# Kernel optimization log

Hardware: AMD Instinct MI355X
Metric: run time of the kernel (lower is better)

Reference implementation:

```python
import jax, jax.numpy as jnp
import numpy as np

D_MODEL = 1024
N_HEADS = 16
D_K = D_MODEL // N_HEADS


def setup_inputs() -> dict:
    key = jax.random.key(0)
    ks = jax.random.split(key, 9)
    s = 0.02
    x = jax.random.normal(ks[0], (2, 2048, D_MODEL), dtype=jnp.float32)
    Wq = jax.random.normal(ks[1], (D_MODEL, D_MODEL), dtype=jnp.float32) * s
    bq = jax.random.normal(ks[2], (D_MODEL,), dtype=jnp.float32) * s
    Wk = jax.random.normal(ks[3], (D_MODEL, D_MODEL), dtype=jnp.float32) * s
    bk = jax.random.normal(ks[4], (D_MODEL,), dtype=jnp.float32) * s
    Wv = jax.random.normal(ks[5], (D_MODEL, D_MODEL), dtype=jnp.float32) * s
    bv = jax.random.normal(ks[6], (D_MODEL,), dtype=jnp.float32) * s
    Wo = jax.random.normal(ks[7], (D_MODEL, D_MODEL), dtype=jnp.float32) * s
    bo = jax.random.normal(ks[8], (D_MODEL,), dtype=jnp.float32) * s
    return {"x": x, "Wq": Wq, "bq": bq, "Wk": Wk, "bk": bk,
            "Wv": Wv, "bv": bv, "Wo": Wo, "bo": bo}


def reference(x, Wq, bq, Wk, bk, Wv, bv, Wo, bo):
    B, S, D = x.shape
    # nn.Linear: y = x @ W.T + b
    q = x @ Wq.T + bq  # [B,S,D]
    k = x @ Wk.T + bk
    v = x @ Wv.T + bv
    # split heads -> [B,H,S,dk]
    q = q.reshape(B, S, N_HEADS, D_K).transpose(0, 2, 1, 3)
    k = k.reshape(B, S, N_HEADS, D_K).transpose(0, 2, 1, 3)
    v = v.reshape(B, S, N_HEADS, D_K).transpose(0, 2, 1, 3)
    scale = 1.0 / jnp.sqrt(jnp.asarray(D_K, dtype=x.dtype))
    scores = jnp.einsum('bhqd,bhkd->bhqk', q, k) * scale  # [B,H,S,S]
    weights = jax.nn.softmax(scores, axis=-1)
    out = jnp.einsum('bhqk,bhkd->bhqd', weights, v)  # [B,H,S,dk]
    concat = out.transpose(0, 2, 1, 3).reshape(B, S, D)
    return concat @ Wo.T + bo
```

## Files before the change

### kernel.cpp

```cpp
#include <hip/hip_runtime.h>

typedef unsigned short ushort_t;
typedef __attribute__((ext_vector_type(8))) __bf16 bf16x8;
typedef __attribute__((ext_vector_type(4))) float floatx4;

#define AS1 __attribute__((address_space(1)))
#define AS3 __attribute__((address_space(3)))

#define D_MODEL 1024
#define NH 16
#define DKH 64
#define SEQ 2048
#define NB 2
#define MTOT (NB * SEQ)

#define QSCALE 0.18033688011112042f

#define OFF_X   0u
#define OFF_WQ  4194304u
#define OFF_BQ  5242880u
#define OFF_WK  5243904u
#define OFF_BK  6292480u
#define OFF_WV  6293504u
#define OFF_BV  7342080u
#define OFF_WO  7343104u
#define OFF_BO  8391680u
#define CVT_TOT 8392704u

__device__ __forceinline__ float bf2f(ushort_t u) {
    union { unsigned u; float f; } v; v.u = ((unsigned)u) << 16; return v.f;
}
__device__ __forceinline__ ushort_t f2bf(float f) {
    union { float f; unsigned u; } v; v.f = f;
    unsigned r = v.u + 0x7FFFu + ((v.u >> 16) & 1u);
    return (ushort_t)(r >> 16);
}
__device__ __forceinline__ unsigned pack2bf(float a, float b) {
    unsigned ua = __float_as_uint(a), ub = __float_as_uint(b);
    ua = ua + 0x7FFFu + ((ua >> 16) & 1u);
    ub = ub + 0x7FFFu + ((ub >> 16) & 1u);
    return __builtin_amdgcn_perm(ub, ua, 0x07060302);
}

__global__ __launch_bounds__(256) void convert_kernel(
    const float* __restrict__ x,  const float* __restrict__ wq, const float* __restrict__ bq_,
    const float* __restrict__ wk, const float* __restrict__ bk_, const float* __restrict__ wv,
    const float* __restrict__ bv_, const float* __restrict__ wo, const float* __restrict__ bo_,
    ushort_t* __restrict__ dst)
{
    const unsigned idx = ((unsigned)blockIdx.x * 256u + threadIdx.x) * 4u;
    if (idx >= CVT_TOT) return;
    const float* src; unsigned off;
    if      (idx < OFF_WQ) { src = x;   off = idx; }
    else if (idx < OFF_BQ) { src = wq;  off = idx - OFF_WQ; }
    else if (idx < OFF_WK) { src = bq_; off = idx - OFF_BQ; }
    else if (idx < OFF_BK) { src = wk;  off = idx - OFF_WK; }
    else if (idx < OFF_WV) { src = bk_; off = idx - OFF_BK; }
    else if (idx < OFF_BV) { src = wv;  off = idx - OFF_WV; }
    else if (idx < OFF_WO) { src = bv_; off = idx - OFF_BV; }
    else if (idx < OFF_BO) { src = wo;  off = idx - OFF_WO; }
    else                   { src = bo_; off = idx - OFF_BO; }
    float4 v = *reinterpret_cast<const float4*>(src + off);
    uint2 p;
    p.x = pack2bf(v.x, v.y);
    p.y = pack2bf(v.z, v.w);
    *reinterpret_cast<uint2*>(dst + idx) = p;
}

__device__ __forceinline__ void gemm_core(
    const ushort_t* __restrict__ X, const ushort_t* __restrict__ W,
    int m0, int n0, ushort_t* As, ushort_t* Bs, floatx4 acc[4][4])
{
    const int tid = threadIdx.x;
    const int lane = tid & 63, wv = tid >> 6;
    const int wm = (wv >> 1) * 64, wn = (wv & 1) * 64;
    const int l15 = lane & 15, quad = lane >> 4;
    const floatx4 z4 = {0.f, 0.f, 0.f, 0.f};
#pragma unroll
    for (int i = 0; i < 4; ++i)
#pragma unroll
        for (int j = 0; j < 4; ++j) acc[i][j] = z4;
    const int lrow = lane >> 2;
    const int lcol = (lane & 3) * 8;
    const ushort_t* gA = X + (size_t)(m0 + lrow) * D_MODEL + lcol;
    const ushort_t* gB = W + (size_t)(n0 + lrow) * D_MODEL + lcol;
    for (int k0 = 0; k0 < D_MODEL; k0 += 32) {
        __syncthreads();
#pragma unroll
        for (int j = 0; j < 2; ++j) {
            const int r0 = (wv * 2 + j) * 16;
            __builtin_amdgcn_global_load_lds(
                (const AS1 unsigned*)(gA + (size_t)r0 * D_MODEL + k0),
                (AS3 unsigned*)(As + r0 * 32), 16, 0, 0);
            __builtin_amdgcn_global_load_lds(
                (const AS1 unsigned*)(gB + (size_t)r0 * D_MODEL + k0),
                (AS3 unsigned*)(Bs + r0 * 32), 16, 0, 0);
        }
        asm volatile("s_waitcnt vmcnt(0)" ::: "memory");
        __syncthreads();
        bf16x8 af[4], bfr[4];
#pragma unroll
        for (int i = 0; i < 4; ++i)
            af[i] = *reinterpret_cast<const bf16x8*>(As + (wm + i * 16 + l15) * 32 + quad * 8);
#pragma unroll
        for (int j = 0; j < 4; ++j)
            bfr[j] = *reinterpret_cast<const bf16x8*>(Bs + (wn + j * 16 + l15) * 32 + quad * 8);
#pragma unroll
        for (int i = 0; i < 4; ++i)
#pragma unroll
            for (int j = 0; j < 4; ++j)
                acc[i][j] = __builtin_amdgcn_mfma_f32_16x16x32_bf16(af[i], bfr[j], acc[i][j], 0, 0, 0);
    }
}

__global__ __launch_bounds__(256, 3) void qkv_kernel(
    const ushort_t* __restrict__ x,
    const ushort_t* __restrict__ Wq, const ushort_t* __restrict__ bq,
    const ushort_t* __restrict__ Wk, const ushort_t* __restrict__ bk,
    const ushort_t* __restrict__ Wv, const ushort_t* __restrict__ bv,
    ushort_t* __restrict__ q_ws, ushort_t* __restrict__ k_ws, ushort_t* __restrict__ vt_ws)
{
    __shared__ __align__(16) ushort_t lds[17408];
    ushort_t* As = lds;
    ushort_t* Bs = lds + 128 * 32;
    const int m0 = blockIdx.x * 128;
    const int which = blockIdx.y >> 3;
    const int n0 = (blockIdx.y & 7) * 128;
    const ushort_t* W    = (which == 0) ? Wq : (which == 1) ? Wk : Wv;
    const ushort_t* bias = (which == 0) ? bq : (which == 1) ? bk : bv;
    floatx4 acc[4][4];
    gemm_core(x, W, m0, n0, As, Bs, acc);
    const int tid = threadIdx.x, lane = tid & 63, wv = tid >> 6;
    const int wm = (wv >> 1) * 64, wn = (wv & 1) * 64;
    const int l15 = lane & 15, quad = lane >> 4;
    const int b0 = m0 >> 11;
    const int s0 = m0 & (SEQ - 1);
    __syncthreads();
    if (which < 2) {
        ushort_t* Ts = lds;
        ushort_t* dst = (which == 0) ? q_ws : k_ws;
        const float scl = (which == 0) ? QSCALE : 1.0f;
#pragma unroll
        for (int j = 0; j < 4; ++j) {
            int coln = wn + j * 16 + l15;
            float bb = bf2f(bias[n0 + coln]);
#pragma unroll
            for (int i = 0; i < 4; ++i)
#pragma unroll
                for (int r = 0; r < 4; ++r) {
                    int rowm = wm + i * 16 + quad * 4 + r;
                    Ts[rowm * 136 + coln] = f2bf((acc[i][j][r] + bb) * scl);
                }
        }
        __syncthreads();
#pragma unroll
        for (int i = 0; i < 8; ++i) {
            int c = tid + 256 * i;
            int rowm = c >> 4, chunk = c & 15;
            float4 v = *reinterpret_cast<const float4*>(Ts + rowm * 136 + chunk * 8);
            int s = s0 + rowm;
            int n = n0 + chunk * 8, h = n >> 6, d = n & 63;
            *reinterpret_cast<float4*>(dst + (((size_t)(b0 * NH + h)) * SEQ + s) * DKH + d) = v;
        }
    } else {
        ushort_t* Ts = lds;
#pragma unroll
        for (int j = 0; j < 4; ++j) {
            int coln = wn + j * 16 + l15;
            float bb = bf2f(bias[n0 + coln]);
#pragma unroll
            for (int i = 0; i < 4; ++i)
#pragma unroll
                for (int r = 0; r < 4; ++r) {
                    int rowm = wm + i * 16 + quad * 4 + r;
                    Ts[coln * 136 + rowm] = f2bf(acc[i][j][r] + bb);
                }
        }
        __syncthreads();
#pragma unroll
        for (int i = 0; i < 8; ++i) {
            int c = tid + 256 * i;
            int nr = c >> 4, mc = (c & 15) * 8;
            float4 v = *reinterpret_cast<const float4*>(Ts + nr * 136 + mc);
            int n = n0 + nr, h = n >> 6, d = n & 63;
            *reinterpret_cast<float4*>(vt_ws + (((size_t)(b0 * NH + h)) * DKH + d) * SEQ + s0 + mc) = v;
        }
    }
}

__global__ __launch_bounds__(512, 4) void attn_kernel(
    const ushort_t* __restrict__ q_ws, const ushort_t* __restrict__ k_ws,
    const ushort_t* __restrict__ vt_ws, ushort_t* __restrict__ concat)
{
    __shared__ __align__(16) ushort_t sm[36864];
    const int qb = blockIdx.x, bh = blockIdx.y;
    const int tid = threadIdx.x;
    const int lane = tid & 63, wv = tid >> 6;
    const int half = wv >> 2, wq = wv & 3;
    const int l15 = lane & 15, quad = lane >> 4;
    const int ht = tid & 255;

    const ushort_t* Qg = q_ws + ((size_t)bh * SEQ + qb * 128) * DKH;
    const ushort_t* Kg = k_ws + ((size_t)bh * SEQ + half * (SEQ / 2)) * DKH;
    const ushort_t* Vg = vt_ws + (size_t)bh * DKH * SEQ + half * (SEQ / 2);

    ushort_t* Ks     = sm + half * 4608;
    ushort_t* VTs    = sm + 9216 + half * 4608;
    ushort_t* Ps     = sm + 18432 + wv * 2304;
    ushort_t* Qstage = sm + 18432;

#pragma unroll
    for (int i = 0; i < 2; ++i) {
        int c = tid + 512 * i;
        int row = c >> 3, col = (c & 7) * 8;
        *reinterpret_cast<float4*>(Qstage + row * 72 + col) =
            *reinterpret_cast<const float4*>(Qg + row * DKH + col);
    }
    __syncthreads();
    bf16x8 aq[2][2];
#pragma unroll
    for (int nt = 0; nt < 2; ++nt)
#pragma unroll
        for (int ks = 0; ks < 2; ++ks)
            aq[nt][ks] = *reinterpret_cast<const bf16x8*>(Qstage + (wq * 32 + nt * 16 + l15) * 72 + ks * 32 + quad * 8);

    const floatx4 z4 = {0.f, 0.f, 0.f, 0.f};
    floatx4 o[2][4];
    float lacc[2] = {0.f, 0.f};
#pragma unroll
    for (int nt = 0; nt < 2; ++nt)
#pragma unroll
        for (int dt = 0; dt < 4; ++dt) o[nt][dt] = z4;

    for (int t = 0; t < 16; ++t) {
        __syncthreads();
#pragma unroll
        for (int i = 0; i < 2; ++i) {
            int c = ht + 256 * i;
            int row = c >> 3, col = (c & 7) * 8;
            *reinterpret_cast<float4*>(Ks + row * 72 + col) =
                *reinterpret_cast<const float4*>(Kg + (size_t)(t * 64 + row) * DKH + col);
            *reinterpret_cast<float4*>(VTs + row * 72 + col) =
                *reinterpret_cast<const float4*>(Vg + (size_t)row * SEQ + t * 64 + col);
        }
        __syncthreads();

        floatx4 st[2][4];
#pragma unroll
        for (int nt = 0; nt < 2; ++nt)
#pragma unroll
            for (int mt = 0; mt < 4; ++mt) st[nt][mt] = z4;
#pragma unroll
        for (int ks = 0; ks < 2; ++ks)
#pragma unroll
            for (int mt = 0; mt < 4; ++mt) {
                bf16x8 akf = *reinterpret_cast<const bf16x8*>(Ks + (mt * 16 + l15) * 72 + ks * 32 + quad * 8);
                st[0][mt] = __builtin_amdgcn_mfma_f32_16x16x32_bf16(akf, aq[0][ks], st[0][mt], 0, 0, 0);
                st[1][mt] = __builtin_amdgcn_mfma_f32_16x16x32_bf16(akf, aq[1][ks], st[1][mt], 0, 0, 0);
            }

#pragma unroll
        for (int nt = 0; nt < 2; ++nt)
#pragma unroll
            for (int mt = 0; mt < 4; ++mt)
#pragma unroll
                for (int r = 0; r < 4; ++r) {
                    float p = exp2f(st[nt][mt][r]);
                    st[nt][mt][r] = p;
                    lacc[nt] += p;
                }
#pragma unroll
        for (int nt = 0; nt < 2; ++nt)
#pragma unroll
            for (int mt = 0; mt < 4; ++mt) {
                uint2 pk;
                pk.x = pack2bf(st[nt][mt][0], st[nt][mt][1]);
                pk.y = pack2bf(st[nt][mt][2], st[nt][mt][3]);
                *reinterpret_cast<uint2*>(Ps + (nt * 16 + l15) * 72 + mt * 16 + quad * 4) = pk;
            }
        asm volatile("s_waitcnt lgkmcnt(0)" ::: "memory");
#pragma unroll
        for (int ks = 0; ks < 2; ++ks) {
            bf16x8 ap0 = *reinterpret_cast<const bf16x8*>(Ps + l15 * 72 + ks * 32 + quad * 8);
            bf16x8 ap1 = *reinterpret_cast<const bf16x8*>(Ps + (16 + l15) * 72 + ks * 32 + quad * 8);
#pragma unroll
            for (int dt = 0; dt < 4; ++dt) {
                bf16x8 bvv = *reinterpret_cast<const bf16x8*>(VTs + (dt * 16 + l15) * 72 + ks * 32 + quad * 8);
                o[0][dt] = __builtin_amdgcn_mfma_f32_16x16x32_bf16(ap0, bvv, o[0][dt], 0, 0, 0);
                o[1][dt] = __builtin_amdgcn_mfma_f32_16x16x32_bf16(ap1, bvv, o[1][dt], 0, 0, 0);
            }
        }
    }
#pragma unroll
    for (int nt = 0; nt < 2; ++nt) {
        lacc[nt] += __shfl_xor(lacc[nt], 16, 64);
        lacc[nt] += __shfl_xor(lacc[nt], 32, 64);
    }
    __syncthreads();
    float* Of = (float*)sm;
    float* lf = Of + 128 * 68;
    if (half == 1) {
#pragma unroll
        for (int nt = 0; nt < 2; ++nt) {
            if (quad == 0) lf[wq * 32 + nt * 16 + l15] = lacc[nt];
#pragma unroll
            for (int r = 0; r < 4; ++r) {
                int row = wq * 32 + nt * 16 + quad * 4 + r;
#pragma unroll
                for (int dt = 0; dt < 4; ++dt)
                    Of[row * 68 + dt * 16 + l15] = o[nt][dt][r];
            }
        }
    }
    __syncthreads();
    if (half == 0) {
        const int b0 = bh >> 4, h = bh & 15;
#pragma unroll
        for (int nt = 0; nt < 2; ++nt) {
            float ltot = lacc[nt] + lf[wq * 32 + nt * 16 + l15];
            float linv = 1.f / ltot;
#pragma unroll
            for (int r = 0; r < 4; ++r) {
                float lB = __shfl(linv, quad * 4 + r, 64);
                int row = wq * 32 + nt * 16 + quad * 4 + r;
                size_t base = ((size_t)(b0 * SEQ + qb * 128 + row)) * D_MODEL + h * DKH;
#pragma unroll
                for (int dt = 0; dt < 4; ++dt) {
                    float sum = o[nt][dt][r] + Of[row * 68 + dt * 16 + l15];
                    concat[base + dt * 16 + l15] = f2bf(sum * lB);
                }
            }
        }
    }
}

__global__ __launch_bounds__(256, 3) void oproj_kernel(
    const ushort_t* __restrict__ cc, const ushort_t* __restrict__ Wo,
    const ushort_t* __restrict__ bo, float* __restrict__ out)
{
    __shared__ __align__(16) ushort_t lds[2 * 128 * 32];
    ushort_t* As = lds;
    ushort_t* Bs = lds + 128 * 32;
    const int m0 = blockIdx.x * 128, n0 = blockIdx.y * 128;
    floatx4 acc[4][4];
    gemm_core(cc, Wo, m0, n0, As, Bs, acc);
    const int tid = threadIdx.x, lane = tid & 63, wv = tid >> 6;
    const int wm = (wv >> 1) * 64, wn = (wv & 1) * 64;
    const int l15 = lane & 15, quad = lane >> 4;
#pragma unroll
    for (int j = 0; j < 4; ++j) {
        int n = n0 + wn + j * 16 + l15;
        float bb = bf2f(bo[n]);
#pragma unroll
        for (int i = 0; i < 4; ++i)
#pragma unroll
            for (int r = 0; r < 4; ++r) {
                int m = m0 + wm + i * 16 + quad * 4 + r;
                out[(size_t)m * D_MODEL + n] = acc[i][j][r] + bb;
            }
    }
}

extern "C" void kernel_launch(void* const* d_in, const int* in_sizes, int n_in,
                              void* d_out, int out_size, void* d_ws, size_t ws_size,
                              hipStream_t stream)
{
    ushort_t* cvt = (ushort_t*)d_ws;
    const ushort_t* xb  = cvt + OFF_X;
    const ushort_t* Wqb = cvt + OFF_WQ;
    const ushort_t* bqb = cvt + OFF_BQ;
    const ushort_t* Wkb = cvt + OFF_WK;
    const ushort_t* bkb = cvt + OFF_BK;
    const ushort_t* Wvb = cvt + OFF_WV;
    const ushort_t* bvb = cvt + OFF_BV;
    const ushort_t* Wob = cvt + OFF_WO;
    const ushort_t* bob = cvt + OFF_BO;
    ushort_t* q_ws   = cvt + CVT_TOT;
    ushort_t* k_ws   = q_ws  + (size_t)MTOT * D_MODEL;
    ushort_t* vt_ws  = k_ws  + (size_t)MTOT * D_MODEL;
    ushort_t* concat = vt_ws + (size_t)MTOT * D_MODEL;

    convert_kernel<<<(CVT_TOT / 1024), 256, 0, stream>>>(
        (const float*)d_in[0], (const float*)d_in[1], (const float*)d_in[2],
        (const float*)d_in[3], (const float*)d_in[4], (const float*)d_in[5],
        (const float*)d_in[6], (const float*)d_in[7], (const float*)d_in[8], cvt);
    qkv_kernel<<<dim3(32, 24), 256, 0, stream>>>(xb, Wqb, bqb, Wkb, bkb, Wvb, bvb, q_ws, k_ws, vt_ws);
    attn_kernel<<<dim3(16, 32), 512, 0, stream>>>(q_ws, k_ws, vt_ws, concat);
    oproj_kernel<<<dim3(32, 8), 256, 0, stream>>>(concat, Wob, bob, (float*)d_out);
}
```

Measured before the change: 210.2 us.

## Keep softmax probabilities in registers, shrink attention blocks, deepen GEMM K-step

Attention now feeds the exponentiated scores straight from the score accumulators into a 16x16x16 MFMA as the B operand with V^T as A, so the LDS round trip for P is gone. Attention blocks shrink to 256 threads and 64 queries with a grid of 32x32, and Q is loaded straight from global memory instead of through LDS staging. The QKV and output-projection GEMMs load a 64-wide K slab per barrier, halving the number of syncs at the cost of twice the LDS per block. The epilogue transposes the partial-output exchange layout so concat writes become packed 4-element stores.

```diff
diff --git a/kernel.cpp b/kernel.cpp
--- a/kernel.cpp
+++ b/kernel.cpp
@@ -2,6 +2,7 @@
 
 typedef unsigned short ushort_t;
 typedef __attribute__((ext_vector_type(8))) __bf16 bf16x8;
+typedef __attribute__((ext_vector_type(4))) short short4v;
 typedef __attribute__((ext_vector_type(4))) float floatx4;
 
 #define AS1 __attribute__((address_space(1)))
@@ -27,6 +28,8 @@
 #define OFF_BO  8391680u
 #define CVT_TOT 8392704u
 
+#define MFMA16(a, b, c) __builtin_amdgcn_mfma_f32_16x16x16bf16_1k((a), (b), (c), 0, 0, 0)
+
 __device__ __forceinline__ float bf2f(ushort_t u) {
     union { unsigned u; float f; } v; v.u = ((unsigned)u) << 16; return v.f;
 }
@@ -40,6 +43,12 @@
     ua = ua + 0x7FFFu + ((ua >> 16) & 1u);
     ub = ub + 0x7FFFu + ((ub >> 16) & 1u);
     return __builtin_amdgcn_perm(ub, ua, 0x07060302);
+}
+__device__ __forceinline__ short4v pack4bf(floatx4 v) {
+    union { uint2 u; short4v s; } cv;
+    cv.u.x = pack2bf(v[0], v[1]);
+    cv.u.y = pack2bf(v[2], v[3]);
+    return cv.s;
 }
 
 __global__ __launch_bounds__(256) void convert_kernel(
@@ -69,7 +78,7 @@
 
 __device__ __forceinline__ void gemm_core(
     const ushort_t* __restrict__ X, const ushort_t* __restrict__ W,
-    int m0, int n0, ushort_t* As, ushort_t* Bs, floatx4 acc[4][4])
+    int m0, int n0, ushort_t* lds, floatx4 acc[4][4])
 {
     const int tid = threadIdx.x;
     const int lane = tid & 63, wv = tid >> 6;
@@ -84,32 +93,43 @@
     const int lcol = (lane & 3) * 8;
     const ushort_t* gA = X + (size_t)(m0 + lrow) * D_MODEL + lcol;
     const ushort_t* gB = W + (size_t)(n0 + lrow) * D_MODEL + lcol;
-    for (int k0 = 0; k0 < D_MODEL; k0 += 32) {
+    for (int k0 = 0; k0 < D_MODEL; k0 += 64) {
         __syncthreads();
 #pragma unroll
         for (int j = 0; j < 2; ++j) {
             const int r0 = (wv * 2 + j) * 16;
             __builtin_amdgcn_global_load_lds(
                 (const AS1 unsigned*)(gA + (size_t)r0 * D_MODEL + k0),
-                (AS3 unsigned*)(As + r0 * 32), 16, 0, 0);
+                (AS3 unsigned*)(lds + r0 * 32), 16, 0, 0);
+            __builtin_amdgcn_global_load_lds(
+                (const AS1 unsigned*)(gA + (size_t)r0 * D_MODEL + k0 + 32),
+                (AS3 unsigned*)(lds + 4096 + r0 * 32), 16, 0, 0);
             __builtin_amdgcn_global_load_lds(
                 (const AS1 unsigned*)(gB + (size_t)r0 * D_MODEL + k0),
-                (AS3 unsigned*)(Bs + r0 * 32), 16, 0, 0);
+                (AS3 unsigned*)(lds + 8192 + r0 * 32), 16, 0, 0);
+            __builtin_amdgcn_global_load_lds(
+                (const AS1 unsigned*)(gB + (size_t)r0 * D_MODEL + k0 + 32),
+                (AS3 unsigned*)(lds + 12288 + r0 * 32), 16, 0, 0);
         }
         asm volatile("s_waitcnt vmcnt(0)" ::: "memory");
         __syncthreads();
-        bf16x8 af[4], bfr[4];
-#pragma unroll
-        for (int i = 0; i < 4; ++i)
-            af[i] = *reinterpret_cast<const bf16x8*>(As + (wm + i * 16 + l15) * 32 + quad * 8);
-#pragma unroll
-        for (int j = 0; j < 4; ++j)
-            bfr[j] = *reinterpret_cast<const bf16x8*>(Bs + (wn + j * 16 + l15) * 32 + quad * 8);
-#pragma unroll
-        for (int i = 0; i < 4; ++i)
+#pragma unroll
+        for (int ks = 0; ks < 2; ++ks) {
+            const ushort_t* A = lds + ks * 4096;
+            const ushort_t* B = lds + 8192 + ks * 4096;
+            bf16x8 af[4], bfr[4];
+#pragma unroll
+            for (int i = 0; i < 4; ++i)
+                af[i] = *reinterpret_cast<const bf16x8*>(A + (wm + i * 16 + l15) * 32 + quad * 8);
 #pragma unroll
             for (int j = 0; j < 4; ++j)
-                acc[i][j] = __builtin_amdgcn_mfma_f32_16x16x32_bf16(af[i], bfr[j], acc[i][j], 0, 0, 0);
+                bfr[j] = *reinterpret_cast<const bf16x8*>(B + (wn + j * 16 + l15) * 32 + quad * 8);
+#pragma unroll
+            for (int i = 0; i < 4; ++i)
+#pragma unroll
+                for (int j = 0; j < 4; ++j)
+                    acc[i][j] = __builtin_amdgcn_mfma_f32_16x16x32_bf16(af[i], bfr[j], acc[i][j], 0, 0, 0);
+        }
     }
 }
 
@@ -121,15 +141,13 @@
     ushort_t* __restrict__ q_ws, ushort_t* __restrict__ k_ws, ushort_t* __restrict__ vt_ws)
 {
     __shared__ __align__(16) ushort_t lds[17408];
-    ushort_t* As = lds;
-    ushort_t* Bs = lds + 128 * 32;
     const int m0 = blockIdx.x * 128;
     const int which = blockIdx.y >> 3;
     const int n0 = (blockIdx.y & 7) * 128;
     const ushort_t* W    = (which == 0) ? Wq : (which == 1) ? Wk : Wv;
     const ushort_t* bias = (which == 0) ? bq : (which == 1) ? bk : bv;
     floatx4 acc[4][4];
-    gemm_core(x, W, m0, n0, As, Bs, acc);
+    gemm_core(x, W, m0, n0, lds, acc);
     const int tid = threadIdx.x, lane = tid & 63, wv = tid >> 6;
     const int wm = (wv >> 1) * 64, wn = (wv & 1) * 64;
     const int l15 = lane & 15, quad = lane >> 4;
@@ -188,45 +206,36 @@
     }
 }
 
-__global__ __launch_bounds__(512, 4) void attn_kernel(
+__global__ __launch_bounds__(256, 4) void attn_kernel(
     const ushort_t* __restrict__ q_ws, const ushort_t* __restrict__ k_ws,
     const ushort_t* __restrict__ vt_ws, ushort_t* __restrict__ concat)
 {
-    __shared__ __align__(16) ushort_t sm[36864];
+    __shared__ __align__(16) ushort_t sm[18432];
     const int qb = blockIdx.x, bh = blockIdx.y;
     const int tid = threadIdx.x;
     const int lane = tid & 63, wv = tid >> 6;
-    const int half = wv >> 2, wq = wv & 3;
+    const int half = wv >> 1, wq = wv & 1;
     const int l15 = lane & 15, quad = lane >> 4;
-    const int ht = tid & 255;
-
-    const ushort_t* Qg = q_ws + ((size_t)bh * SEQ + qb * 128) * DKH;
+    const int ht = tid & 127;
+
+    const ushort_t* Qg = q_ws + ((size_t)bh * SEQ + qb * 64) * DKH;
     const ushort_t* Kg = k_ws + ((size_t)bh * SEQ + half * (SEQ / 2)) * DKH;
     const ushort_t* Vg = vt_ws + (size_t)bh * DKH * SEQ + half * (SEQ / 2);
 
-    ushort_t* Ks     = sm + half * 4608;
-    ushort_t* VTs    = sm + 9216 + half * 4608;
-    ushort_t* Ps     = sm + 18432 + wv * 2304;
-    ushort_t* Qstage = sm + 18432;
-
-#pragma unroll
-    for (int i = 0; i < 2; ++i) {
-        int c = tid + 512 * i;
-        int row = c >> 3, col = (c & 7) * 8;
-        *reinterpret_cast<float4*>(Qstage + row * 72 + col) =
-            *reinterpret_cast<const float4*>(Qg + row * DKH + col);
-    }
-    __syncthreads();
+    ushort_t* Ks  = sm + half * 4608;
+    ushort_t* VTs = sm + 9216 + half * 4608;
+
     bf16x8 aq[2][2];
 #pragma unroll
     for (int nt = 0; nt < 2; ++nt)
 #pragma unroll
         for (int ks = 0; ks < 2; ++ks)
-            aq[nt][ks] = *reinterpret_cast<const bf16x8*>(Qstage + (wq * 32 + nt * 16 + l15) * 72 + ks * 32 + quad * 8);
+            aq[nt][ks] = *reinterpret_cast<const bf16x8*>(
+                Qg + (size_t)(wq * 32 + nt * 16 + l15) * DKH + ks * 32 + quad * 8);
 
     const floatx4 z4 = {0.f, 0.f, 0.f, 0.f};
     floatx4 o[2][4];
-    float lacc[2] = {0.f, 0.f};
+    floatx4 la4[2] = {z4, z4};
 #pragma unroll
     for (int nt = 0; nt < 2; ++nt)
 #pragma unroll
@@ -235,8 +244,8 @@
     for (int t = 0; t < 16; ++t) {
         __syncthreads();
 #pragma unroll
-        for (int i = 0; i < 2; ++i) {
-            int c = ht + 256 * i;
+        for (int i = 0; i < 4; ++i) {
+            int c = ht + 128 * i;
             int row = c >> 3, col = (c & 7) * 8;
             *reinterpret_cast<float4*>(Ks + row * 72 + col) =
                 *reinterpret_cast<const float4*>(Kg + (size_t)(t * 64 + row) * DKH + col);
@@ -259,57 +268,47 @@
                 st[1][mt] = __builtin_amdgcn_mfma_f32_16x16x32_bf16(akf, aq[1][ks], st[1][mt], 0, 0, 0);
             }
 
+        short4v pb[2][4];
 #pragma unroll
         for (int nt = 0; nt < 2; ++nt)
 #pragma unroll
-            for (int mt = 0; mt < 4; ++mt)
-#pragma unroll
-                for (int r = 0; r < 4; ++r) {
-                    float p = exp2f(st[nt][mt][r]);
-                    st[nt][mt][r] = p;
-                    lacc[nt] += p;
-                }
-#pragma unroll
-        for (int nt = 0; nt < 2; ++nt)
-#pragma unroll
             for (int mt = 0; mt < 4; ++mt) {
-                uint2 pk;
-                pk.x = pack2bf(st[nt][mt][0], st[nt][mt][1]);
-                pk.y = pack2bf(st[nt][mt][2], st[nt][mt][3]);
-                *reinterpret_cast<uint2*>(Ps + (nt * 16 + l15) * 72 + mt * 16 + quad * 4) = pk;
-            }
-        asm volatile("s_waitcnt lgkmcnt(0)" ::: "memory");
-#pragma unroll
-        for (int ks = 0; ks < 2; ++ks) {
-            bf16x8 ap0 = *reinterpret_cast<const bf16x8*>(Ps + l15 * 72 + ks * 32 + quad * 8);
-            bf16x8 ap1 = *reinterpret_cast<const bf16x8*>(Ps + (16 + l15) * 72 + ks * 32 + quad * 8);
+#pragma unroll
+                for (int r = 0; r < 4; ++r) st[nt][mt][r] = exp2f(st[nt][mt][r]);
+                la4[nt] += st[nt][mt];
+                pb[nt][mt] = pack4bf(st[nt][mt]);
+            }
+
+#pragma unroll
+        for (int mt = 0; mt < 4; ++mt)
 #pragma unroll
             for (int dt = 0; dt < 4; ++dt) {
-                bf16x8 bvv = *reinterpret_cast<const bf16x8*>(VTs + (dt * 16 + l15) * 72 + ks * 32 + quad * 8);
-                o[0][dt] = __builtin_amdgcn_mfma_f32_16x16x32_bf16(ap0, bvv, o[0][dt], 0, 0, 0);
-                o[1][dt] = __builtin_amdgcn_mfma_f32_16x16x32_bf16(ap1, bvv, o[1][dt], 0, 0, 0);
-            }
-        }
-    }
+                short4v av = *reinterpret_cast<const short4v*>(VTs + (dt * 16 + l15) * 72 + mt * 16 + quad * 4);
+                o[0][dt] = MFMA16(av, pb[0][mt], o[0][dt]);
+                o[1][dt] = MFMA16(av, pb[1][mt], o[1][dt]);
+            }
+    }
+    float lsum[2];
 #pragma unroll
     for (int nt = 0; nt < 2; ++nt) {
-        lacc[nt] += __shfl_xor(lacc[nt], 16, 64);
-        lacc[nt] += __shfl_xor(lacc[nt], 32, 64);
+        float s = la4[nt][0] + la4[nt][1] + la4[nt][2] + la4[nt][3];
+        s += __shfl_xor(s, 16, 64);
+        s += __shfl_xor(s, 32, 64);
+        lsum[nt] = s;
     }
     __syncthreads();
     float* Of = (float*)sm;
-    float* lf = Of + 128 * 68;
+    float* lf = Of + 64 * 65;
     if (half == 1) {
 #pragma unroll
         for (int nt = 0; nt < 2; ++nt) {
-            if (quad == 0) lf[wq * 32 + nt * 16 + l15] = lacc[nt];
-#pragma unroll
-            for (int r = 0; r < 4; ++r) {
-                int row = wq * 32 + nt * 16 + quad * 4 + r;
-#pragma unroll
-                for (int dt = 0; dt < 4; ++dt)
-                    Of[row * 68 + dt * 16 + l15] = o[nt][dt][r];
-            }
+            int q = wq * 32 + nt * 16 + l15;
+            if (quad == 0) lf[q] = lsum[nt];
+#pragma unroll
+            for (int dt = 0; dt < 4; ++dt)
+#pragma unroll
+                for (int r = 0; r < 4; ++r)
+                    Of[(dt * 16 + quad * 4 + r) * 65 + q] = o[nt][dt][r];
         }
     }
     __syncthreads();
@@ -317,18 +316,19 @@
         const int b0 = bh >> 4, h = bh & 15;
 #pragma unroll
         for (int nt = 0; nt < 2; ++nt) {
-            float ltot = lacc[nt] + lf[wq * 32 + nt * 16 + l15];
-            float linv = 1.f / ltot;
-#pragma unroll
-            for (int r = 0; r < 4; ++r) {
-                float lB = __shfl(linv, quad * 4 + r, 64);
-                int row = wq * 32 + nt * 16 + quad * 4 + r;
-                size_t base = ((size_t)(b0 * SEQ + qb * 128 + row)) * D_MODEL + h * DKH;
-#pragma unroll
-                for (int dt = 0; dt < 4; ++dt) {
-                    float sum = o[nt][dt][r] + Of[row * 68 + dt * 16 + l15];
-                    concat[base + dt * 16 + l15] = f2bf(sum * lB);
-                }
+            int q = wq * 32 + nt * 16 + l15;
+            float linv = 1.f / (lsum[nt] + lf[q]);
+            size_t base = ((size_t)(b0 * SEQ + qb * 64 + q)) * D_MODEL + h * DKH;
+#pragma unroll
+            for (int dt = 0; dt < 4; ++dt) {
+                float f0 = (o[nt][dt][0] + Of[(dt * 16 + quad * 4 + 0) * 65 + q]) * linv;
+                float f1 = (o[nt][dt][1] + Of[(dt * 16 + quad * 4 + 1) * 65 + q]) * linv;
+                float f2 = (o[nt][dt][2] + Of[(dt * 16 + quad * 4 + 2) * 65 + q]) * linv;
+                float f3 = (o[nt][dt][3] + Of[(dt * 16 + quad * 4 + 3) * 65 + q]) * linv;
+                uint2 pk;
+                pk.x = pack2bf(f0, f1);
+                pk.y = pack2bf(f2, f3);
+                *reinterpret_cast<uint2*>(concat + base + dt * 16 + quad * 4) = pk;
             }
         }
     }
@@ -338,12 +338,10 @@
     const ushort_t* __restrict__ cc, const ushort_t* __restrict__ Wo,
     const ushort_t* __restrict__ bo, float* __restrict__ out)
 {
-    __shared__ __align__(16) ushort_t lds[2 * 128 * 32];
-    ushort_t* As = lds;
-    ushort_t* Bs = lds + 128 * 32;
+    __shared__ __align__(16) ushort_t lds[4 * 128 * 32];
     const int m0 = blockIdx.x * 128, n0 = blockIdx.y * 128;
     floatx4 acc[4][4];
-    gemm_core(cc, Wo, m0, n0, As, Bs, acc);
+    gemm_core(cc, Wo, m0, n0, lds, acc);
     const int tid = threadIdx.x, lane = tid & 63, wv = tid >> 6;
     const int wm = (wv >> 1) * 64, wn = (wv & 1) * 64;
     const int l15 = lane & 15, quad = lane >> 4;
@@ -385,6 +383,6 @@
         (const float*)d_in[3], (const float*)d_in[4], (const float*)d_in[5],
         (const float*)d_in[6], (const float*)d_in[7], (const float*)d_in[8], cvt);
     qkv_kernel<<<dim3(32, 24), 256, 0, stream>>>(xb, Wqb, bqb, Wkb, bkb, Wvb, bvb, q_ws, k_ws, vt_ws);
-    attn_kernel<<<dim3(16, 32), 512, 0, stream>>>(q_ws, k_ws, vt_ws, concat);
+    attn_kernel<<<dim3(32, 32), 256, 0, stream>>>(q_ws, k_ws, vt_ws, concat);
     oproj_kernel<<<dim3(32, 8), 256, 0, stream>>>(concat, Wob, bob, (float*)d_out);
 }
```

After: 226.3 us. 7.7% more time.
